# Kernel optimization log

Measured on AMD Instinct MI355X. Metric: run time of the kernel, lower is better.

Reference implementation:

```python
import jax, jax.numpy as jnp
import numpy as np

Q_MIN, Q_MAX = -128.0, 127.0  # int8 range (brevitas signed, narrow_range=False)


def ste_round(x):
    # straight-through round (matches brevitas training semantics)
    return x + jax.lax.stop_gradient(jnp.round(x) - x)


def fake_quant(x, s):
    # per-tensor int8 quant-dequant: clamp(round(x/s), -128, 127) * s
    return jnp.clip(ste_round(x / s), Q_MIN, Q_MAX) * s


def conv2d(x, w):
    # NCHW x OIHW, stride 1, VALID padding (kernel (3,3), no padding arg in source)
    return jax.lax.conv_general_dilated(
        x, w, window_strides=(1, 1), padding='VALID',
        dimension_numbers=('NCHW', 'OIHW', 'NCHW'))


def setup_inputs() -> dict:
    key = jax.random.key(0)
    k = jax.random.split(key, 5)
    x = jax.random.normal(k[0], (32, 5, 512, 512), jnp.float32)
    w1 = jax.random.normal(k[1], (10, 5, 3, 3), jnp.float32) * 0.1
    b1 = jax.random.normal(k[2], (10,), jnp.float32) * 0.1
    w2 = jax.random.normal(k[3], (10, 10, 3, 3), jnp.float32) * 0.1
    b2 = jax.random.normal(k[4], (10,), jnp.float32) * 0.1
    # fixed-point (power-of-two) per-tensor scales
    s_in = jnp.full((1,), 2.0 ** -4, jnp.float32)
    s_w1 = jnp.full((1,), 2.0 ** -7, jnp.float32)
    s_o1 = jnp.full((1,), 2.0 ** -4, jnp.float32)
    s_w2 = jnp.full((1,), 2.0 ** -7, jnp.float32)
    s_o2 = jnp.full((1,), 2.0 ** -4, jnp.float32)
    return {"x": x, "w1": w1, "b1": b1, "w2": w2, "b2": b2,
            "s_in": s_in, "s_w1": s_w1, "s_o1": s_o1, "s_w2": s_w2, "s_o2": s_o2}


def reference(x, w1, b1, w2, b2, s_in, s_w1, s_o1, s_w2, s_o2):
    # QuantIdentity(Int8ActPerTensorFixedPoint)
    xq = fake_quant(x, s_in)
    # QuantConv2d #1: weight quant, bias quant (scale = in_scale*w_scale), output quant
    w1q = fake_quant(w1, s_w1)
    b1q = fake_quant(b1, s_in * s_w1)
    y = conv2d(xq, w1q) + b1q[None, :, None, None]  # [32,10,510,510]
    yq = fake_quant(y, s_o1)
    # QuantConv2d #2
    w2q = fake_quant(w2, s_w2)
    b2q = fake_quant(b2, s_o1 * s_w2)
    z = conv2d(yq, w2q) + b2q[None, :, None, None]  # [32,10,508,508]
    return fake_quant(z, s_o2)
```

## Files before the change

kernel.cpp:

```cpp
#include <hip/hip_runtime.h>


#define XQ_OFF   8192
#define YQ_OFF   41951488ULL

typedef int v4i __attribute__((ext_vector_type(4)));

__device__ __forceinline__ float qclamp(float v) {
    return fminf(fmaxf(v, -128.0f), 127.0f);
}

__device__ __forceinline__ int alignb(int hi, int lo, int sh) {
#if __has_builtin(__builtin_amdgcn_alignbyte)
    return __builtin_amdgcn_alignbyte(hi, lo, sh);
#else
    return (int)((((unsigned long long)(unsigned)hi << 32) | (unsigned)lo) >> (8 * sh));
#endif
}

__global__ __launch_bounds__(256) void prep_kernel(
    const float* __restrict__ w1, const float* __restrict__ b1,
    const float* __restrict__ w2, const float* __restrict__ b2,
    const float* __restrict__ s_in, const float* __restrict__ s_w1,
    const float* __restrict__ s_o1, const float* __restrict__ s_w2,
    const float* __restrict__ s_o2,
    float* __restrict__ consts, int* __restrict__ wA1, int* __restrict__ b1i,
    int* __restrict__ wA2, int* __restrict__ b2i)
{
    int t = threadIdx.x;
    float si = s_in[0], sw1 = s_w1[0], so1 = s_o1[0], sw2 = s_w2[0], so2 = s_o2[0];
    if (t == 0) {
        consts[0] = 1.0f / si;
        consts[1] = (si * sw1) / so1;
        consts[2] = (so1 * sw2) / so2;
        consts[3] = so2;
    }
    {
        int l = t >> 2, r = t & 3;
        int g = l >> 4, m = l & 15;
        int d = 4 * g + r;
        int val = 0;
        if (d < 15 && m < 10) {
            int c = d / 3, kh = d % 3;
            const float* src = w1 + (((m * 5 + c) * 3 + kh) * 3);
            int q0 = (int)qclamp(rintf(src[0] / sw1));
            int q1 = (int)qclamp(rintf(src[1] / sw1));
            int q2 = (int)qclamp(rintf(src[2] / sw1));
            val = (q0 & 255) | ((q1 & 255) << 8) | ((q2 & 255) << 16);
        }
        wA1[t] = val;
    }
    for (int i = t; i < 512; i += 256) {
        int l = i >> 3, r = i & 7;
        int g = l >> 4, m = l & 15;
        int f = r >> 2;
        int d = f * 16 + 4 * g + (r & 3);
        int val = 0;
        if (d < 30 && m < 10) {
            int c = d / 3, kh = d % 3;
            const float* src = w2 + (((m * 10 + c) * 3 + kh) * 3);
            int q0 = (int)qclamp(rintf(src[0] / sw2));
            int q1 = (int)qclamp(rintf(src[1] / sw2));
            int q2 = (int)qclamp(rintf(src[2] / sw2));
            val = (q0 & 255) | ((q1 & 255) << 8) | ((q2 & 255) << 16);
        }
        wA2[i] = val;
    }
    if (t < 16) {
        b1i[t] = (t < 10) ? (int)qclamp(rintf(b1[t] / (si * sw1))) : 0;
        b2i[t] = (t < 10) ? (int)qclamp(rintf(b2[t] / (so1 * sw2))) : 0;
    }
}

__global__ __launch_bounds__(256) void quant_x_kernel(
    const float4* __restrict__ x, const float* __restrict__ consts,
    int* __restrict__ xq, int n4)
{
    int i = blockIdx.x * 256 + threadIdx.x;
    if (i >= n4) return;
    float inv = consts[0];
    float4 v = x[i];
    int q0 = (int)qclamp(rintf(v.x * inv));
    int q1 = (int)qclamp(rintf(v.y * inv));
    int q2 = (int)qclamp(rintf(v.z * inv));
    int q3 = (int)qclamp(rintf(v.w * inv));
    xq[i] = (q0 & 255) | ((q1 & 255) << 8) | ((q2 & 255) << 16) | (q3 << 24);
}

__global__ __launch_bounds__(256) void conv1_mfma(
    const signed char* __restrict__ xq, const int* __restrict__ wA,
    const int* __restrict__ bi, const float* __restrict__ consts,
    signed char* __restrict__ yq)
{
    int tid = threadIdx.x;
    int b = blockIdx.x;
    int rc = b & 31, wt = (b >> 5) & 1, n = b >> 6;
    int oh0 = rc * 16;
    int rows = 510 - oh0; if (rows > 16) rows = 16;
    int ow0 = wt << 8;

    __shared__ int lds[4 * 5 * 72];

    int lane = tid & 63;
    int w = tid >> 6;
    int g = lane >> 4, m = lane & 15;
    int sh = m & 3;
    int wcol = w * 64;

    v4i a = ((const v4i*)wA)[lane];
    v4i cinit;
    #pragma unroll
    for (int r = 0; r < 4; ++r) cinit[r] = bi[4 * g + r];

    int khv[4], inv[4];
    #pragma unroll
    for (int j = 0; j < 4; ++j) {
        int d = 4 * g + j;
        int c = 0, kh = 0;
        if (d < 15) { c = d / 3; kh = d % 3; }
        khv[j] = kh;
        inv[j] = c * 72 + ((wcol + (m & ~3)) >> 2);
    }

    const signed char* src = xq + (size_t)n * (5 * 512 * 512);
    float cr1 = consts[1];

    #define STAGE1(ih_) do {                                                 \
        int ih = (ih_);                                                      \
        int slot = ih & 3;                                                   \
        _Pragma("unroll")                                                    \
        for (int pass = 0; pass < 2; ++pass) {                               \
            int j = tid + pass * 256;                                        \
            if (j < 340) {                                                   \
                int c = j / 68;                                              \
                int off = j - c * 68;                                        \
                int col = ow0 + (off << 2);                                  \
                if (col > 508) col = 508;                                    \
                lds[(slot * 5 + c) * 72 + off] =                             \
                    *(const int*)(src + c * 262144 + ih * 512 + col);        \
            }                                                                \
        }                                                                    \
    } while (0)

    STAGE1(oh0);
    STAGE1(oh0 + 1);

    for (int i = 0; i < rows; ++i) {
        int oh = oh0 + i;
        STAGE1(oh + 2);
        __syncthreads();

        int rsl[4];
        #pragma unroll
        for (int j = 0; j < 4; ++j)
            rsl[j] = ((oh + khv[j]) & 3) * 360 + inv[j];

        size_t sb = (size_t)(n * 10) * (510 * 512) + (size_t)oh * 512
                  + (size_t)(ow0 + wcol + m);
        #pragma unroll
        for (int nt = 0; nt < 4; ++nt) {
            v4i bb;
            #pragma unroll
            for (int j = 0; j < 4; ++j) {
                const int* p = lds + rsl[j] + nt * 4;
                int u0 = p[0], u1 = p[1];
                bb[j] = alignb(u1, u0, sh);
            }
            v4i acc = __builtin_amdgcn_mfma_i32_16x16x64_i8(a, bb, cinit, 0, 0, 0);
            int colv = ow0 + wcol + nt * 16 + m;
            bool cv = colv < 510;
            #pragma unroll
            for (int r = 0; r < 4; ++r) {
                int oc = 4 * g + r;
                if (oc < 10 && cv) {
                    int q = (int)qclamp(rintf((float)acc[r] * cr1));
                    yq[sb + nt * 16 + (size_t)oc * (510 * 512)] = (signed char)q;
                }
            }
        }
        __syncthreads();
    }
    #undef STAGE1
}

__global__ __launch_bounds__(256) void conv2_mfma(
    const signed char* __restrict__ yq, const int* __restrict__ wA,
    const int* __restrict__ bi, const float* __restrict__ consts,
    float* __restrict__ out)
{
    int tid = threadIdx.x;
    int b = blockIdx.x;
    int rc = b & 31, wt = (b >> 5) & 1, n = b >> 6;
    int oh0 = rc * 16;
    int rows = 508 - oh0; if (rows > 16) rows = 16;
    int ow0 = wt << 8;

    __shared__ int lds[4 * 10 * 72];

    int lane = tid & 63;
    int w = tid >> 6;
    int g = lane >> 4, m = lane & 15;
    int sh = m & 3;
    int wcol = w * 64;

    const v4i* wA4 = (const v4i*)wA;
    v4i a0 = wA4[lane * 2 + 0];
    v4i a1 = wA4[lane * 2 + 1];
    v4i cinit;
    #pragma unroll
    for (int r = 0; r < 4; ++r) cinit[r] = bi[4 * g + r];

    int khv[8], inv[8];
    #pragma unroll
    for (int s = 0; s < 8; ++s) {
        int d = (s >> 2) * 16 + 4 * g + (s & 3);
        int c = 0, kh = 0;
        if (d < 30) { c = d / 3; kh = d % 3; }
        khv[s] = kh;
        inv[s] = c * 72 + ((wcol + (m & ~3)) >> 2);
    }

    const signed char* src = yq + (size_t)n * (10 * 510 * 512);
    float cr2 = consts[2];
    float so  = consts[3];

    #define STAGE2(ih_) do {                                                 \
        int ih = (ih_);                                                      \
        int slot = ih & 3;                                                   \
        _Pragma("unroll")                                                    \
        for (int pass = 0; pass < 3; ++pass) {                               \
            int j = tid + pass * 256;                                        \
            if (j < 680) {                                                   \
                int c = j / 68;                                              \
                int off = j - c * 68;                                        \
                int col = ow0 + (off << 2);                                  \
                if (col > 508) col = 508;                                    \
                lds[(slot * 10 + c) * 72 + off] =                            \
                    *(const int*)(src + c * (510 * 512) + ih * 512 + col);   \
            }                                                                \
        }                                                                    \
    } while (0)

    STAGE2(oh0);
    STAGE2(oh0 + 1);

    for (int i = 0; i < rows; ++i) {
        int oh = oh0 + i;
        STAGE2(oh + 2);
        __syncthreads();

        int rsl[8];
        #pragma unroll
        for (int s = 0; s < 8; ++s)
            rsl[s] = ((oh + khv[s]) & 3) * 720 + inv[s];

        size_t ob = (size_t)(n * 10) * (508 * 508) + (size_t)oh * 508;
        #pragma unroll
        for (int nt = 0; nt < 4; ++nt) {
            v4i bb0, bb1;
            #pragma unroll
            for (int s = 0; s < 4; ++s) {
                const int* p = lds + rsl[s] + nt * 4;
                int u0 = p[0], u1 = p[1];
                bb0[s] = alignb(u1, u0, sh);
            }
            #pragma unroll
            for (int s = 4; s < 8; ++s) {
                const int* p = lds + rsl[s] + nt * 4;
                int u0 = p[0], u1 = p[1];
                bb1[s - 4] = alignb(u1, u0, sh);
            }
            v4i acc = __builtin_amdgcn_mfma_i32_16x16x64_i8(a0, bb0, cinit, 0, 0, 0);
            acc = __builtin_amdgcn_mfma_i32_16x16x64_i8(a1, bb1, acc, 0, 0, 0);
            int colv = ow0 + wcol + nt * 16 + m;
            bool cv = colv < 508;
            #pragma unroll
            for (int r = 0; r < 4; ++r) {
                int oc = 4 * g + r;
                if (oc < 10 && cv) {
                    float v = qclamp(rintf((float)acc[r] * cr2)) * so;
                    out[ob + (size_t)oc * (508 * 508) + colv] = v;
                }
            }
        }
        __syncthreads();
    }
    #undef STAGE2
}

extern "C" void kernel_launch(void* const* d_in, const int* in_sizes, int n_in,
                              void* d_out, int out_size, void* d_ws, size_t ws_size,
                              hipStream_t stream) {
    const float* x    = (const float*)d_in[0];
    const float* w1   = (const float*)d_in[1];
    const float* b1   = (const float*)d_in[2];
    const float* w2   = (const float*)d_in[3];
    const float* b2   = (const float*)d_in[4];
    const float* s_in = (const float*)d_in[5];
    const float* s_w1 = (const float*)d_in[6];
    const float* s_o1 = (const float*)d_in[7];
    const float* s_w2 = (const float*)d_in[8];
    const float* s_o2 = (const float*)d_in[9];

    char* ws = (char*)d_ws;
    float* consts = (float*)ws;
    int* wA1 = (int*)(ws + 256);
    int* b1i = (int*)(ws + 1280);
    int* wA2 = (int*)(ws + 2048);
    int* b2i = (int*)(ws + 4096);
    signed char* xqb = (signed char*)(ws + XQ_OFF);
    signed char* yqb = (signed char*)(ws + YQ_OFF);

    prep_kernel<<<1, 256, 0, stream>>>(w1, b1, w2, b2, s_in, s_w1, s_o1, s_w2, s_o2,
                                       consts, wA1, b1i, wA2, b2i);

    int n4 = 32 * 5 * 512 * 512 / 4;
    quant_x_kernel<<<(n4 + 255) / 256, 256, 0, stream>>>(
        (const float4*)x, consts, (int*)xqb, n4);

    conv1_mfma<<<2048, 256, 0, stream>>>(xqb, wA1, b1i, consts, yqb);

    conv2_mfma<<<2048, 256, 0, stream>>>(yqb, wA2, b2i, consts, (float*)d_out);
}
```

Baseline: 608.5 us.

## Fuse input quantization into conv1 and stage four rows per barrier with register prefetch

Removes the separate quant_x kernel: conv1 now reads float x directly and quantizes and packs it into LDS, which avoids writing and re-reading the int8 copy of x. Both convs switch to 32-row tiles (half as many blocks) with a 10-slot LDS ring. Each step loads the next four rows into registers while MFMA work runs and syncs once per four rows instead of once per row. This adds register pressure and more LDS per block, which may lower occupancy, and halo reloads are amortized over taller tiles.

```diff
diff --git a/kernel.cpp b/kernel.cpp
--- a/kernel.cpp
+++ b/kernel.cpp
@@ -1,7 +1,6 @@
 #include <hip/hip_runtime.h>
 
 
-#define XQ_OFF   8192
 #define YQ_OFF   41951488ULL
 
 typedef int v4i __attribute__((ext_vector_type(4)));
@@ -16,6 +15,14 @@
 #else
     return (int)((((unsigned long long)(unsigned)hi << 32) | (unsigned)lo) >> (8 * sh));
 #endif
+}
+
+__device__ __forceinline__ int pack4(float4 v, float s) {
+    int q0 = (int)qclamp(rintf(v.x * s));
+    int q1 = (int)qclamp(rintf(v.y * s));
+    int q2 = (int)qclamp(rintf(v.z * s));
+    int q3 = (int)qclamp(rintf(v.w * s));
+    return (q0 & 255) | ((q1 & 255) << 8) | ((q2 & 255) << 16) | (q3 << 24);
 }
 
 __global__ __launch_bounds__(256) void prep_kernel(
@@ -72,34 +79,18 @@
     }
 }
 
-__global__ __launch_bounds__(256) void quant_x_kernel(
-    const float4* __restrict__ x, const float* __restrict__ consts,
-    int* __restrict__ xq, int n4)
-{
-    int i = blockIdx.x * 256 + threadIdx.x;
-    if (i >= n4) return;
-    float inv = consts[0];
-    float4 v = x[i];
-    int q0 = (int)qclamp(rintf(v.x * inv));
-    int q1 = (int)qclamp(rintf(v.y * inv));
-    int q2 = (int)qclamp(rintf(v.z * inv));
-    int q3 = (int)qclamp(rintf(v.w * inv));
-    xq[i] = (q0 & 255) | ((q1 & 255) << 8) | ((q2 & 255) << 16) | (q3 << 24);
-}
-
 __global__ __launch_bounds__(256) void conv1_mfma(
-    const signed char* __restrict__ xq, const int* __restrict__ wA,
+    const float* __restrict__ x, const int* __restrict__ wA,
     const int* __restrict__ bi, const float* __restrict__ consts,
     signed char* __restrict__ yq)
 {
     int tid = threadIdx.x;
     int b = blockIdx.x;
-    int rc = b & 31, wt = (b >> 5) & 1, n = b >> 6;
-    int oh0 = rc * 16;
-    int rows = 510 - oh0; if (rows > 16) rows = 16;
+    int rc = b & 15, wt = (b >> 4) & 1, n = b >> 5;
+    int oh0 = rc * 32;
     int ow0 = wt << 8;
 
-    __shared__ int lds[4 * 5 * 72];
+    __shared__ int lds[10 * 360];
 
     int lane = tid & 63;
     int w = tid >> 6;
@@ -112,75 +103,112 @@
     #pragma unroll
     for (int r = 0; r < 4; ++r) cinit[r] = bi[4 * g + r];
 
-    int khv[4], inv[4];
+    int khv[4], invv[4];
     #pragma unroll
     for (int j = 0; j < 4; ++j) {
         int d = 4 * g + j;
         int c = 0, kh = 0;
         if (d < 15) { c = d / 3; kh = d % 3; }
         khv[j] = kh;
-        inv[j] = c * 72 + ((wcol + (m & ~3)) >> 2);
-    }
-
-    const signed char* src = xq + (size_t)n * (5 * 512 * 512);
+        invv[j] = c * 72 + ((wcol + (m & ~3)) >> 2);
+    }
+
+    float qs  = consts[0];
     float cr1 = consts[1];
-
-    #define STAGE1(ih_) do {                                                 \
-        int ih = (ih_);                                                      \
-        int slot = ih & 3;                                                   \
-        _Pragma("unroll")                                                    \
-        for (int pass = 0; pass < 2; ++pass) {                               \
-            int j = tid + pass * 256;                                        \
-            if (j < 340) {                                                   \
-                int c = j / 68;                                              \
-                int off = j - c * 68;                                        \
-                int col = ow0 + (off << 2);                                  \
-                if (col > 508) col = 508;                                    \
-                lds[(slot * 5 + c) * 72 + off] =                             \
-                    *(const int*)(src + c * 262144 + ih * 512 + col);        \
-            }                                                                \
-        }                                                                    \
-    } while (0)
-
-    STAGE1(oh0);
-    STAGE1(oh0 + 1);
-
-    for (int i = 0; i < rows; ++i) {
-        int oh = oh0 + i;
-        STAGE1(oh + 2);
+    const float* xb = x + (size_t)n * (5 * 512 * 512);
+
+    int rl_[6], lb_[6], go_[6]; bool va_[6];
+    #pragma unroll
+    for (int i = 0; i < 6; ++i) {
+        int j = tid + i * 256;
+        va_[i] = j < 1360;
+        int jj = va_[i] ? j : 0;
+        int rl = jj / 340, rem = jj - rl * 340;
+        int c = rem / 68, off = rem - c * 68;
+        int col = ow0 + off * 4; if (col > 508) col = 508;
+        rl_[i] = rl;
+        lb_[i] = c * 72 + off;
+        go_[i] = c * 262144 + col;
+    }
+
+    #pragma unroll
+    for (int i = 0; i < 8; ++i) {
+        int j = tid + i * 256;
+        if (j < 2040) {
+            int rl = j / 340, rem = j - rl * 340;
+            int c = rem / 68, off = rem - c * 68;
+            int col = ow0 + off * 4; if (col > 508) col = 508;
+            int ih = oh0 + rl; if (ih > 511) ih = 511;
+            float4 v = *(const float4*)(xb + (size_t)c * 262144 + ih * 512 + col);
+            lds[rl * 360 + c * 72 + off] = pack4(v, qs);
+        }
+    }
+    __syncthreads();
+
+    int s_off = 0;
+    for (int k = 0; k < 8; ++k) {
+        int oh = oh0 + 4 * k;
+        bool do_stage = k < 7;
+
+        float4 sreg[6];
+        if (do_stage) {
+            int ihb = oh + 6;
+            #pragma unroll
+            for (int i = 0; i < 6; ++i) {
+                int ih = ihb + rl_[i]; if (ih > 511) ih = 511;
+                if (va_[i])
+                    sreg[i] = *(const float4*)(xb + go_[i] + (size_t)ih * 512);
+            }
+        }
+
+        #pragma unroll
+        for (int r = 0; r < 4; ++r) {
+            int ohr = oh + r;
+            if (ohr >= 510) break;
+            int sofr = s_off + r;
+            int rsl[4];
+            #pragma unroll
+            for (int j = 0; j < 4; ++j) {
+                int t = sofr + khv[j]; if (t >= 10) t -= 10;
+                rsl[j] = t * 360 + invv[j];
+            }
+            size_t sb = (size_t)(n * 10) * (510 * 512) + (size_t)ohr * 512
+                      + (size_t)(ow0 + wcol + m);
+            #pragma unroll
+            for (int nt = 0; nt < 4; ++nt) {
+                v4i bb;
+                #pragma unroll
+                for (int j = 0; j < 4; ++j) {
+                    const int* p = lds + rsl[j] + nt * 4;
+                    int u0 = p[0], u1 = p[1];
+                    bb[j] = alignb(u1, u0, sh);
+                }
+                v4i acc = __builtin_amdgcn_mfma_i32_16x16x64_i8(a, bb, cinit, 0, 0, 0);
+                int colv = ow0 + wcol + nt * 16 + m;
+                bool cv = colv < 510;
+                #pragma unroll
+                for (int rr = 0; rr < 4; ++rr) {
+                    int oc = 4 * g + rr;
+                    if (oc < 10 && cv) {
+                        int q = (int)qclamp(rintf((float)acc[rr] * cr1));
+                        yq[sb + nt * 16 + (size_t)oc * (510 * 512)] = (signed char)q;
+                    }
+                }
+            }
+        }
+
+        if (do_stage) {
+            #pragma unroll
+            for (int i = 0; i < 6; ++i) {
+                if (va_[i]) {
+                    int t = s_off + 6 + rl_[i]; if (t >= 10) t -= 10;
+                    lds[t * 360 + lb_[i]] = pack4(sreg[i], qs);
+                }
+            }
+        }
         __syncthreads();
-
-        int rsl[4];
-        #pragma unroll
-        for (int j = 0; j < 4; ++j)
-            rsl[j] = ((oh + khv[j]) & 3) * 360 + inv[j];
-
-        size_t sb = (size_t)(n * 10) * (510 * 512) + (size_t)oh * 512
-                  + (size_t)(ow0 + wcol + m);
-        #pragma unroll
-        for (int nt = 0; nt < 4; ++nt) {
-            v4i bb;
-            #pragma unroll
-            for (int j = 0; j < 4; ++j) {
-                const int* p = lds + rsl[j] + nt * 4;
-                int u0 = p[0], u1 = p[1];
-                bb[j] = alignb(u1, u0, sh);
-            }
-            v4i acc = __builtin_amdgcn_mfma_i32_16x16x64_i8(a, bb, cinit, 0, 0, 0);
-            int colv = ow0 + wcol + nt * 16 + m;
-            bool cv = colv < 510;
-            #pragma unroll
-            for (int r = 0; r < 4; ++r) {
-                int oc = 4 * g + r;
-                if (oc < 10 && cv) {
-                    int q = (int)qclamp(rintf((float)acc[r] * cr1));
-                    yq[sb + nt * 16 + (size_t)oc * (510 * 512)] = (signed char)q;
-                }
-            }
-        }
-        __syncthreads();
-    }
-    #undef STAGE1
+        s_off += 4; if (s_off >= 10) s_off -= 10;
+    }
 }
 
 __global__ __launch_bounds__(256) void conv2_mfma(
@@ -190,12 +218,11 @@
 {
     int tid = threadIdx.x;
     int b = blockIdx.x;
-    int rc = b & 31, wt = (b >> 5) & 1, n = b >> 6;
-    int oh0 = rc * 16;
-    int rows = 508 - oh0; if (rows > 16) rows = 16;
+    int rc = b & 15, wt = (b >> 4) & 1, n = b >> 5;
+    int oh0 = rc * 32;
     int ow0 = wt << 8;
 
-    __shared__ int lds[4 * 10 * 72];
+    __shared__ int lds[10 * 720];
 
     int lane = tid & 63;
     int w = tid >> 6;
@@ -210,82 +237,120 @@
     #pragma unroll
     for (int r = 0; r < 4; ++r) cinit[r] = bi[4 * g + r];
 
-    int khv[8], inv[8];
+    int khv[8], invv[8];
     #pragma unroll
     for (int s = 0; s < 8; ++s) {
         int d = (s >> 2) * 16 + 4 * g + (s & 3);
         int c = 0, kh = 0;
         if (d < 30) { c = d / 3; kh = d % 3; }
         khv[s] = kh;
-        inv[s] = c * 72 + ((wcol + (m & ~3)) >> 2);
-    }
-
-    const signed char* src = yq + (size_t)n * (10 * 510 * 512);
+        invv[s] = c * 72 + ((wcol + (m & ~3)) >> 2);
+    }
+
+    const signed char* yb = yq + (size_t)n * (10 * 510 * 512);
     float cr2 = consts[2];
     float so  = consts[3];
 
-    #define STAGE2(ih_) do {                                                 \
-        int ih = (ih_);                                                      \
-        int slot = ih & 3;                                                   \
-        _Pragma("unroll")                                                    \
-        for (int pass = 0; pass < 3; ++pass) {                               \
-            int j = tid + pass * 256;                                        \
-            if (j < 680) {                                                   \
-                int c = j / 68;                                              \
-                int off = j - c * 68;                                        \
-                int col = ow0 + (off << 2);                                  \
-                if (col > 508) col = 508;                                    \
-                lds[(slot * 10 + c) * 72 + off] =                            \
-                    *(const int*)(src + c * (510 * 512) + ih * 512 + col);   \
-            }                                                                \
-        }                                                                    \
-    } while (0)
-
-    STAGE2(oh0);
-    STAGE2(oh0 + 1);
-
-    for (int i = 0; i < rows; ++i) {
-        int oh = oh0 + i;
-        STAGE2(oh + 2);
+    int rl_[11], lb_[11], go_[11]; bool va_[11];
+    #pragma unroll
+    for (int i = 0; i < 11; ++i) {
+        int j = tid + i * 256;
+        va_[i] = j < 2720;
+        int jj = va_[i] ? j : 0;
+        int rl = jj / 680, rem = jj - rl * 680;
+        int c = rem / 68, off = rem - c * 68;
+        int col = ow0 + off * 4; if (col > 508) col = 508;
+        rl_[i] = rl;
+        lb_[i] = c * 72 + off;
+        go_[i] = c * 261120 + col;
+    }
+
+    #pragma unroll
+    for (int i = 0; i < 16; ++i) {
+        int j = tid + i * 256;
+        if (j < 4080) {
+            int rl = j / 680, rem = j - rl * 680;
+            int c = rem / 68, off = rem - c * 68;
+            int col = ow0 + off * 4; if (col > 508) col = 508;
+            int ih = oh0 + rl; if (ih > 509) ih = 509;
+            lds[rl * 720 + c * 72 + off] =
+                *(const int*)(yb + (size_t)c * 261120 + (size_t)ih * 512 + col);
+        }
+    }
+    __syncthreads();
+
+    int valid = 508 - oh0; if (valid > 32) valid = 32;
+    int nph = (valid + 3) >> 2;
+    int s_off = 0;
+    for (int k = 0; k < nph; ++k) {
+        int oh = oh0 + 4 * k;
+        bool do_stage = (k + 1) < nph;
+
+        int sreg[11];
+        if (do_stage) {
+            int ihb = oh + 6;
+            #pragma unroll
+            for (int i = 0; i < 11; ++i) {
+                int ih = ihb + rl_[i]; if (ih > 509) ih = 509;
+                if (va_[i])
+                    sreg[i] = *(const int*)(yb + go_[i] + (size_t)ih * 512);
+            }
+        }
+
+        #pragma unroll
+        for (int r = 0; r < 4; ++r) {
+            int ohr = oh + r;
+            if (ohr >= 508) break;
+            int sofr = s_off + r;
+            int rsl[8];
+            #pragma unroll
+            for (int s = 0; s < 8; ++s) {
+                int t = sofr + khv[s]; if (t >= 10) t -= 10;
+                rsl[s] = t * 720 + invv[s];
+            }
+            size_t ob = (size_t)(n * 10) * (508 * 508) + (size_t)ohr * 508;
+            #pragma unroll
+            for (int nt = 0; nt < 4; ++nt) {
+                v4i bb0, bb1;
+                #pragma unroll
+                for (int s = 0; s < 4; ++s) {
+                    const int* p = lds + rsl[s] + nt * 4;
+                    int u0 = p[0], u1 = p[1];
+                    bb0[s] = alignb(u1, u0, sh);
+                }
+                #pragma unroll
+                for (int s = 4; s < 8; ++s) {
+                    const int* p = lds + rsl[s] + nt * 4;
+                    int u0 = p[0], u1 = p[1];
+                    bb1[s - 4] = alignb(u1, u0, sh);
+                }
+                v4i acc = __builtin_amdgcn_mfma_i32_16x16x64_i8(a0, bb0, cinit, 0, 0, 0);
+                acc = __builtin_amdgcn_mfma_i32_16x16x64_i8(a1, bb1, acc, 0, 0, 0);
+                int colv = ow0 + wcol + nt * 16 + m;
+                bool cv = colv < 508;
+                #pragma unroll
+                for (int rr = 0; rr < 4; ++rr) {
+                    int oc = 4 * g + rr;
+                    if (oc < 10 && cv) {
+                        float v = qclamp(rintf((float)acc[rr] * cr2)) * so;
+                        out[ob + (size_t)oc * (508 * 508) + colv] = v;
+                    }
+                }
+            }
+        }
+
+        if (do_stage) {
+            #pragma unroll
+            for (int i = 0; i < 11; ++i) {
+                if (va_[i]) {
+                    int t = s_off + 6 + rl_[i]; if (t >= 10) t -= 10;
+                    lds[t * 720 + lb_[i]] = sreg[i];
+                }
+            }
+        }
         __syncthreads();
-
-        int rsl[8];
-        #pragma unroll
-        for (int s = 0; s < 8; ++s)
-            rsl[s] = ((oh + khv[s]) & 3) * 720 + inv[s];
-
-        size_t ob = (size_t)(n * 10) * (508 * 508) + (size_t)oh * 508;
-        #pragma unroll
-        for (int nt = 0; nt < 4; ++nt) {
-            v4i bb0, bb1;
-            #pragma unroll
-            for (int s = 0; s < 4; ++s) {
-                const int* p = lds + rsl[s] + nt * 4;
-                int u0 = p[0], u1 = p[1];
-                bb0[s] = alignb(u1, u0, sh);
-            }
-            #pragma unroll
-            for (int s = 4; s < 8; ++s) {
-                const int* p = lds + rsl[s] + nt * 4;
-                int u0 = p[0], u1 = p[1];
-                bb1[s - 4] = alignb(u1, u0, sh);
-            }
-            v4i acc = __builtin_amdgcn_mfma_i32_16x16x64_i8(a0, bb0, cinit, 0, 0, 0);
-            acc = __builtin_amdgcn_mfma_i32_16x16x64_i8(a1, bb1, acc, 0, 0, 0);
-            int colv = ow0 + wcol + nt * 16 + m;
-            bool cv = colv < 508;
-            #pragma unroll
-            for (int r = 0; r < 4; ++r) {
-                int oc = 4 * g + r;
-                if (oc < 10 && cv) {
-                    float v = qclamp(rintf((float)acc[r] * cr2)) * so;
-                    out[ob + (size_t)oc * (508 * 508) + colv] = v;
-                }
-            }
-        }
-        __syncthreads();
-    }
-    #undef STAGE2
+        s_off += 4; if (s_off >= 10) s_off -= 10;
+    }
 }
 
 extern "C" void kernel_launch(void* const* d_in, const int* in_sizes, int n_in,
@@ -308,17 +373,12 @@
     int* b1i = (int*)(ws + 1280);
     int* wA2 = (int*)(ws + 2048);
     int* b2i = (int*)(ws + 4096);
-    signed char* xqb = (signed char*)(ws + XQ_OFF);
     signed char* yqb = (signed char*)(ws + YQ_OFF);
 
     prep_kernel<<<1, 256, 0, stream>>>(w1, b1, w2, b2, s_in, s_w1, s_o1, s_w2, s_o2,
                                        consts, wA1, b1i, wA2, b2i);
 
-    int n4 = 32 * 5 * 512 * 512 / 4;
-    quant_x_kernel<<<(n4 + 255) / 256, 256, 0, stream>>>(
-        (const float4*)x, consts, (int*)xqb, n4);
-
-    conv1_mfma<<<2048, 256, 0, stream>>>(xqb, wA1, b1i, consts, yqb);
-
-    conv2_mfma<<<2048, 256, 0, stream>>>(yqb, wA2, b2i, consts, (float*)d_out);
-}
+    conv1_mfma<<<1024, 256, 0, stream>>>(x, wA1, b1i, consts, yqb);
+
+    conv2_mfma<<<1024, 256, 0, stream>>>(yqb, wA2, b2i, consts, (float*)d_out);
+}
```

Result: faster. 588.3 us (-3.3%).
